# Kernel optimization log

Hardware: AMD Instinct MI355X
Metric: run time of the kernel (lower is better)

The kernel has to match this reference:

```python
import jax, jax.numpy as jnp
import numpy as np

EPS = 1e-5
CG_GROUPS = 4
CG_ALPHA = 2.0

def conv3x3(x, w, stride=1):
    # x: [N,C,H,W], w: [O,I,3,3], padding=1
    return jax.lax.conv_general_dilated(
        x, w, window_strides=(stride, stride), padding=((1, 1), (1, 1)),
        dimension_numbers=('NCHW', 'OIHW', 'NCHW'))

def qconv_cg(x, w, theta):
    # Conditional-gated conv (CGNet-style, wbit=abit=32 -> no quantization):
    # base partial sum from first C/cg_groups input channels, remainder gated
    # by soft sigmoid decision on (Yp - per-channel threshold).
    cin = x.shape[1]
    base = cin // CG_GROUPS  # 64 base channels
    yp = conv3x3(x[:, :base], w[:, :base])          # base partial sum [N,O,H,W]
    yr = conv3x3(x[:, base:], w[:, base:])          # remainder partial sum
    d = jax.nn.sigmoid(CG_ALPHA * (yp - theta[None, :, None, None]))
    return yp + d * yr

def bn(x, gamma, beta, mean, var):
    # inference-mode BatchNorm2d
    inv = gamma * jax.lax.rsqrt(var + EPS)
    return x * inv[None, :, None, None] + (beta - mean * inv)[None, :, None, None]

def setup_inputs() -> dict:
    key = jax.random.key(0)
    k0, k1, k2 = jax.random.split(key, 3)
    C = 256
    x = jax.random.normal(k0, (16, C, 56, 56), jnp.float32)
    scale = 1.0 / np.sqrt(C * 9)
    w_a = jax.random.normal(k1, (C, C, 3, 3), jnp.float32) * scale
    w_b = jax.random.normal(k2, (C, C, 3, 3), jnp.float32) * scale
    z = jnp.zeros((C,), jnp.float32)
    o = jnp.ones((C,), jnp.float32)
    return dict(x=x,
                w_a=w_a, theta_a=z, gamma_a=o, beta_a=z, mean_a=z, var_a=o,
                w_b=w_b, theta_b=z, gamma_b=o, beta_b=z, mean_b=z, var_b=o)

def reference(x, w_a, theta_a, gamma_a, beta_a, mean_a, var_a,
              w_b, theta_b, gamma_b, beta_b, mean_b, var_b):
    h = jax.nn.relu(bn(qconv_cg(x, w_a, theta_a), gamma_a, beta_a, mean_a, var_a))
    h = bn(qconv_cg(h, w_b, theta_b), gamma_b, beta_b, mean_b, var_b)
    return jax.nn.relu(x + h)  # identity residual (downsample=None)
```

## Files before the change

kernel.cpp:

```cpp
#include <hip/hip_runtime.h>
#include <hip/hip_bf16.h>
#include <cstdint>
#include <cstddef>


typedef __attribute__((ext_vector_type(8))) short bf16x8;
typedef __attribute__((ext_vector_type(4))) float f32x4;
typedef __attribute__((ext_vector_type(8))) unsigned short u16x8;

#define HP 58
#define WP 58
#define CIN 256
#define NIMG 16

__device__ __forceinline__ unsigned short f2bf(float f) {
  unsigned int u = __float_as_uint(f);
  u += 0x7fffu + ((u >> 16) & 1u);
  return (unsigned short)(u >> 16);
}

#define GLOAD16(gp, lp)                                                        \
  __builtin_amdgcn_global_load_lds(                                            \
      (const __attribute__((address_space(1))) void*)(gp),                     \
      (__attribute__((address_space(3))) void*)(lp), 16, 0, 0)

__global__ void zero_borders(unsigned short* __restrict__ pad) {
  int b = blockIdx.x;
  int img = b / 58, yp = b - img * 58;
  int tid = threadIdx.x;
  u16x8 z = {0, 0, 0, 0, 0, 0, 0, 0};
  unsigned short* row = pad + ((size_t)(img * HP + yp)) * WP * CIN;
  if (yp == 0 || yp == HP - 1) {
    for (int i = tid; i < WP * CIN / 8; i += 256) ((u16x8*)row)[i] = z;
  } else {
    if (tid < 32) ((u16x8*)row)[tid] = z;
    else if (tid < 64) ((u16x8*)row)[(WP - 1) * CIN / 8 + tid - 32] = z;
  }
}

__global__ void prep_w(const float* __restrict__ wa, const float* __restrict__ wb,
                       unsigned short* __restrict__ bta, unsigned short* __restrict__ btb) {
  int id = blockIdx.x * 256 + threadIdx.x;
  const float* w = (id < 65536) ? wa : wb;
  unsigned short* bt = (id < 65536) ? bta : btb;
  int oi = id & 65535;
  float v[9];
#pragma unroll
  for (int t = 0; t < 9; ++t) v[t] = w[(size_t)oi * 9 + t];
#pragma unroll
  for (int t = 0; t < 9; ++t) bt[(size_t)t * 65536 + oi] = f2bf(v[t]);
}

__global__ void prep_x(const float* __restrict__ x, unsigned short* __restrict__ xpad) {
  __shared__ float ld[56 * 65];
  int b = blockIdx.x;
  int img = b / 56, y = b - img * 56;
  int tid = threadIdx.x;
  for (int cb = 0; cb < 4; ++cb) {
    __syncthreads();
#pragma unroll
    for (int it = 0; it < 14; ++it) {
      int i = tid + it * 256;
      int cl = i / 56, xx = i - cl * 56;
      ld[xx * 65 + cl] = x[((size_t)(img * 256 + cb * 64 + cl) * 56 + y) * 56 + xx];
    }
    __syncthreads();
#pragma unroll
    for (int it = 0; it < 14; ++it) {
      int j = tid + it * 256;
      int xx = j >> 6, c = j & 63;
      xpad[((size_t)((img * HP) + (y + 1)) * WP + (xx + 1)) * CIN + cb * 64 + c] =
          f2bf(ld[xx * 65 + c]);
    }
  }
}

template <int LAYER>
__global__ __launch_bounds__(256, 2)
void conv_cg(const unsigned short* __restrict__ inp,
             const unsigned short* __restrict__ Bt,
             const float* __restrict__ theta,
             const float* __restrict__ gammav,
             const float* __restrict__ betav,
             const float* __restrict__ meanv,
             const float* __restrict__ varv,
             unsigned short* __restrict__ hout,
             const float* __restrict__ xres,
             float* __restrict__ dout)
{
  __shared__ alignas(16) char smem[64 * 129 * 4];
  unsigned short* sA = (unsigned short*)smem;
  unsigned short* sB = (unsigned short*)(smem + 8192);
  float* sep = (float*)smem;

  const int tid = threadIdx.x;
  const int lane = tid & 63;
  const int wid = tid >> 6;
  const int wm = wid >> 1, wn = wid & 1;
  const int l15 = lane & 15, l4 = lane >> 4;
  const int srow = lane >> 3;
  const int sslot = lane & 7;

  int bx = blockIdx.x;
  const int ob = bx & 1; bx >>= 1;
  const int img = bx / 49;
  const int r2 = bx - img * 49;
  const int ty = r2 / 7, tx = r2 - ty * 7;
  const int y0 = ty * 8 + 1, x0 = tx * 8 + 1;

  const size_t img_base = (size_t)img * (HP * WP * CIN);

  f32x4 acc[2][4], ypv[2][4];
  const f32x4 fzero = {0.f, 0.f, 0.f, 0.f};
#pragma unroll
  for (int i = 0; i < 2; ++i)
#pragma unroll
    for (int j = 0; j < 4; ++j) acc[i][j] = fzero;

  for (int phase = 0; phase < 2; ++phase) {
    const int cb_lo = phase ? 1 : 0;
    const int cb_hi = phase ? 4 : 1;
    for (int tap = 0; tap < 9; ++tap) {
      const int dy = tap / 3 - 1, dx = tap - (tap / 3) * 3 - 1;
      for (int cb = cb_lo; cb < cb_hi; ++cb) {
#pragma unroll
        for (int it = 0; it < 2; ++it) {
          int chunk = wid * 2 + it;
          int row = chunk * 8 + srow;
          int ry = row >> 3, rx = row & 7;
          int gy = y0 + ry + dy, gx = x0 + rx + dx;
          int slot = sslot ^ (row & 7);
          const unsigned short* src =
              inp + img_base + ((size_t)(gy * WP + gx)) * CIN + cb * 64 + slot * 8;
          GLOAD16(src, sA + chunk * 512);
        }
#pragma unroll
        for (int it = 0; it < 4; ++it) {
          int chunk = wid * 4 + it;
          int o_l = chunk * 8 + srow;
          int slot = sslot ^ (o_l & 7);
          const unsigned short* src =
              Bt + ((size_t)(tap * 256 + ob * 128 + o_l)) * 256 + cb * 64 + slot * 8;
          GLOAD16(src, sB + chunk * 512);
        }
        __syncthreads();
#pragma unroll
        for (int ks = 0; ks < 2; ++ks) {
          bf16x8 av[2], bv[4];
#pragma unroll
          for (int mi = 0; mi < 2; ++mi) {
            int row = wm * 32 + mi * 16 + l15;
            int sl = (ks * 4 + l4) ^ (row & 7);
            av[mi] = *(const bf16x8*)(sA + row * 64 + sl * 8);
          }
#pragma unroll
          for (int ni = 0; ni < 4; ++ni) {
            int row = wn * 64 + ni * 16 + l15;
            int sl = (ks * 4 + l4) ^ (row & 7);
            bv[ni] = *(const bf16x8*)(sB + row * 64 + sl * 8);
          }
#pragma unroll
          for (int mi = 0; mi < 2; ++mi)
#pragma unroll
            for (int ni = 0; ni < 4; ++ni)
              acc[mi][ni] = __builtin_amdgcn_mfma_f32_16x16x32_bf16(
                  av[mi], bv[ni], acc[mi][ni], 0, 0, 0);
        }
        __syncthreads();
      }
    }
    if (phase == 0) {
#pragma unroll
      for (int i = 0; i < 2; ++i)
#pragma unroll
        for (int j = 0; j < 4; ++j) { ypv[i][j] = acc[i][j]; acc[i][j] = fzero; }
    }
  }

  float th[4], sc[4], bi[4];
#pragma unroll
  for (int ni = 0; ni < 4; ++ni) {
    int o = ob * 128 + wn * 64 + ni * 16 + l15;
    th[ni] = theta[o];
    float inv = gammav[o] * rsqrtf(varv[o] + 1e-5f);
    sc[ni] = inv;
    bi[ni] = betav[o] - meanv[o] * inv;
  }
#pragma unroll
  for (int mi = 0; mi < 2; ++mi)
#pragma unroll
    for (int ni = 0; ni < 4; ++ni) {
      int colL = wn * 64 + ni * 16 + l15;
#pragma unroll
      for (int q = 0; q < 4; ++q) {
        int m = wm * 32 + mi * 16 + l4 * 4 + q;
        float yp = ypv[mi][ni][q], yr = acc[mi][ni][q];
        float d = 1.f / (1.f + __expf(-2.f * (yp - th[ni])));
        float v = (yp + d * yr) * sc[ni] + bi[ni];
        if (LAYER == 1) v = fmaxf(v, 0.f);
        sep[m * 129 + colL] = v;
      }
    }
  __syncthreads();

  if (LAYER == 1) {
#pragma unroll
    for (int it = 0; it < 4; ++it) {
      int j = tid + it * 256;
      int p = j >> 4, o8 = (j & 15) * 8;
      int ry = p >> 3, rx = p & 7;
      u16x8 tv;
#pragma unroll
      for (int e = 0; e < 8; ++e) tv[e] = f2bf(sep[p * 129 + o8 + e]);
      unsigned short* dst =
          hout + img_base + ((size_t)((y0 + ry) * WP + (x0 + rx))) * CIN + ob * 128 + o8;
      *(u16x8*)dst = tv;
    }
  } else {
#pragma unroll
    for (int it = 0; it < 4; ++it) {
      int j = tid + it * 256;
      int o = j >> 3, ry = j & 7;
      int oc = ob * 128 + o;
      size_t gb = ((size_t)((img * 256 + oc) * 56 + (y0 - 1 + ry))) * 56 + (x0 - 1);
      const float4 xa = *(const float4*)(xres + gb);
      const float4 xb = *(const float4*)(xres + gb + 4);
      float4 ra, rb;
      ra.x = fmaxf(xa.x + sep[(ry * 8 + 0) * 129 + o], 0.f);
      ra.y = fmaxf(xa.y + sep[(ry * 8 + 1) * 129 + o], 0.f);
      ra.z = fmaxf(xa.z + sep[(ry * 8 + 2) * 129 + o], 0.f);
      ra.w = fmaxf(xa.w + sep[(ry * 8 + 3) * 129 + o], 0.f);
      rb.x = fmaxf(xb.x + sep[(ry * 8 + 4) * 129 + o], 0.f);
      rb.y = fmaxf(xb.y + sep[(ry * 8 + 5) * 129 + o], 0.f);
      rb.z = fmaxf(xb.z + sep[(ry * 8 + 6) * 129 + o], 0.f);
      rb.w = fmaxf(xb.w + sep[(ry * 8 + 7) * 129 + o], 0.f);
      *(float4*)(dout + gb) = ra;
      *(float4*)(dout + gb + 4) = rb;
    }
  }
}

extern "C" void kernel_launch(void* const* d_in, const int* in_sizes, int n_in,
                              void* d_out, int out_size, void* d_ws, size_t ws_size,
                              hipStream_t stream) {
  const float* x    = (const float*)d_in[0];
  const float* w_a  = (const float*)d_in[1];
  const float* th_a = (const float*)d_in[2];
  const float* ga_a = (const float*)d_in[3];
  const float* be_a = (const float*)d_in[4];
  const float* mu_a = (const float*)d_in[5];
  const float* va_a = (const float*)d_in[6];
  const float* w_b  = (const float*)d_in[7];
  const float* th_b = (const float*)d_in[8];
  const float* ga_b = (const float*)d_in[9];
  const float* be_b = (const float*)d_in[10];
  const float* mu_b = (const float*)d_in[11];
  const float* va_b = (const float*)d_in[12];
  float* out = (float*)d_out;

  const size_t PAD_BYTES = (size_t)NIMG * HP * WP * CIN * 2;
  char* ws = (char*)d_ws;
  unsigned short* xpad = (unsigned short*)ws;
  unsigned short* hpad = (unsigned short*)(ws + 27558912);
  unsigned short* bta  = (unsigned short*)(ws + 2 * 27558912);
  unsigned short* btb  = (unsigned short*)(ws + 2 * 27558912 + 1179648);
  (void)PAD_BYTES; (void)ws_size; (void)in_sizes; (void)n_in; (void)out_size;

  hipLaunchKernelGGL(zero_borders, dim3(NIMG * HP), dim3(256), 0, stream, xpad);
  hipLaunchKernelGGL(zero_borders, dim3(NIMG * HP), dim3(256), 0, stream, hpad);
  hipLaunchKernelGGL(prep_w, dim3(512), dim3(256), 0, stream, w_a, w_b, bta, btb);
  hipLaunchKernelGGL(prep_x, dim3(NIMG * 56), dim3(256), 0, stream, x, xpad);

  hipLaunchKernelGGL((conv_cg<1>), dim3(NIMG * 49 * 2), dim3(256), 0, stream,
                     xpad, bta, th_a, ga_a, be_a, mu_a, va_a,
                     hpad, (const float*)nullptr, (float*)nullptr);
  hipLaunchKernelGGL((conv_cg<2>), dim3(NIMG * 49 * 2), dim3(256), 0, stream,
                     hpad, btb, th_b, ga_b, be_b, mu_b, va_b,
                     (unsigned short*)nullptr, x, out);
}
```

Before: 350.2 us.

## Stage halo input tile once per channel block and double-buffer weights per tap

The conv kernel is restructured so each wave owns one 8x8 pixel tile. It loads a 10x10 halo patch per 64-channel block into LDS once and reuses it across all 9 taps. Before, the input patch was reloaded for every tap. Each block of 4 waves shares a 64-output-channel weight slice, staged per tap with double buffering so the next tap's weights load while MFMAs run. The weight layout is reordered to match, and x-buffer border zeroing is merged into prep_x, removing one launch. In exchange it uses much more LDS (about 66 KB per block), holds 32 accumulator vectors per lane which lowers occupancy, and launches fewer blocks.

```diff
diff --git a/kernel.cpp b/kernel.cpp
--- a/kernel.cpp
+++ b/kernel.cpp
@@ -44,34 +44,60 @@
   const float* w = (id < 65536) ? wa : wb;
   unsigned short* bt = (id < 65536) ? bta : btb;
   int oi = id & 65535;
+  int o = oi >> 8, i = oi & 255;
+  int cb = i >> 6, c = i & 63;
   float v[9];
 #pragma unroll
   for (int t = 0; t < 9; ++t) v[t] = w[(size_t)oi * 9 + t];
 #pragma unroll
-  for (int t = 0; t < 9; ++t) bt[(size_t)t * 65536 + oi] = f2bf(v[t]);
+  for (int t = 0; t < 9; ++t)
+    bt[((size_t)((t * 4 + cb) * 256 + o)) * 64 + c] = f2bf(v[t]);
 }
 
 __global__ void prep_x(const float* __restrict__ x, unsigned short* __restrict__ xpad) {
   __shared__ float ld[56 * 65];
   int b = blockIdx.x;
-  int img = b / 56, y = b - img * 56;
+  int img = b / 58, y = b - img * 58;
   int tid = threadIdx.x;
+  unsigned short* row = xpad + ((size_t)(img * HP + y)) * WP * CIN;
+  u16x8 z = {0, 0, 0, 0, 0, 0, 0, 0};
+  if (y == 0 || y == HP - 1) {
+#pragma unroll
+    for (int it = 0; it < 8; ++it) {
+      int i = it * 256 + tid;
+      if (i < WP * CIN / 8) ((u16x8*)row)[i] = z;
+    }
+    return;
+  }
+  if (tid < 32) ((u16x8*)row)[tid] = z;
+  else if (tid < 64) ((u16x8*)row)[(WP - 1) * CIN / 8 + tid - 32] = z;
+  int ys = y - 1;
   for (int cb = 0; cb < 4; ++cb) {
     __syncthreads();
 #pragma unroll
     for (int it = 0; it < 14; ++it) {
       int i = tid + it * 256;
       int cl = i / 56, xx = i - cl * 56;
-      ld[xx * 65 + cl] = x[((size_t)(img * 256 + cb * 64 + cl) * 56 + y) * 56 + xx];
+      ld[xx * 65 + cl] = x[((size_t)(img * 256 + cb * 64 + cl) * 56 + ys) * 56 + xx];
     }
     __syncthreads();
 #pragma unroll
     for (int it = 0; it < 14; ++it) {
       int j = tid + it * 256;
       int xx = j >> 6, c = j & 63;
-      xpad[((size_t)((img * HP) + (y + 1)) * WP + (xx + 1)) * CIN + cb * 64 + c] =
-          f2bf(ld[xx * 65 + c]);
-    }
+      row[(xx + 1) * CIN + cb * 64 + c] = f2bf(ld[xx * 65 + c]);
+    }
+  }
+}
+
+__device__ __forceinline__ void stage_b(const unsigned short* __restrict__ cbase,
+                                        unsigned short* dst, int wid, int lane) {
+#pragma unroll
+  for (int it = 0; it < 2; ++it) {
+    int d = (wid * 2 + it) * 64 + lane;
+    int o = d >> 3, s = d & 7;
+    const unsigned short* src = cbase + o * 64 + ((s ^ (o & 7)) << 3);
+    GLOAD16(src, dst + (wid * 2 + it) * 512);
   }
 }
 
@@ -88,154 +114,154 @@
              const float* __restrict__ xres,
              float* __restrict__ dout)
 {
-  __shared__ alignas(16) char smem[64 * 129 * 4];
-  unsigned short* sA = (unsigned short*)smem;
-  unsigned short* sB = (unsigned short*)(smem + 8192);
-  float* sep = (float*)smem;
-
+  __shared__ alignas(16) char smem[67584];
   const int tid = threadIdx.x;
   const int lane = tid & 63;
   const int wid = tid >> 6;
-  const int wm = wid >> 1, wn = wid & 1;
   const int l15 = lane & 15, l4 = lane >> 4;
-  const int srow = lane >> 3;
-  const int sslot = lane & 7;
 
   int bx = blockIdx.x;
-  const int ob = bx & 1; bx >>= 1;
-  const int img = bx / 49;
-  const int r2 = bx - img * 49;
-  const int ty = r2 / 7, tx = r2 - ty * 7;
+  const int oq = bx & 3;
+  const int pxg = bx >> 2;
+  const int tile = pxg * 4 + wid;
+  const int img = tile / 49;
+  const int rr = tile - img * 49;
+  const int ty = rr / 7, tx = rr - ty * 7;
   const int y0 = ty * 8 + 1, x0 = tx * 8 + 1;
-
   const size_t img_base = (size_t)img * (HP * WP * CIN);
 
-  f32x4 acc[2][4], ypv[2][4];
-  const f32x4 fzero = {0.f, 0.f, 0.f, 0.f};
-#pragma unroll
-  for (int i = 0; i < 2; ++i)
-#pragma unroll
-    for (int j = 0; j < 4; ++j) acc[i][j] = fzero;
-
-  for (int phase = 0; phase < 2; ++phase) {
-    const int cb_lo = phase ? 1 : 0;
-    const int cb_hi = phase ? 4 : 1;
-    for (int tap = 0; tap < 9; ++tap) {
-      const int dy = tap / 3 - 1, dx = tap - (tap / 3) * 3 - 1;
-      for (int cb = cb_lo; cb < cb_hi; ++cb) {
-#pragma unroll
-        for (int it = 0; it < 2; ++it) {
-          int chunk = wid * 2 + it;
-          int row = chunk * 8 + srow;
-          int ry = row >> 3, rx = row & 7;
-          int gy = y0 + ry + dy, gx = x0 + rx + dx;
-          int slot = sslot ^ (row & 7);
-          const unsigned short* src =
-              inp + img_base + ((size_t)(gy * WP + gx)) * CIN + cb * 64 + slot * 8;
-          GLOAD16(src, sA + chunk * 512);
-        }
-#pragma unroll
-        for (int it = 0; it < 4; ++it) {
-          int chunk = wid * 4 + it;
-          int o_l = chunk * 8 + srow;
-          int slot = sslot ^ (o_l & 7);
-          const unsigned short* src =
-              Bt + ((size_t)(tap * 256 + ob * 128 + o_l)) * 256 + cb * 64 + slot * 8;
-          GLOAD16(src, sB + chunk * 512);
-        }
-        __syncthreads();
-#pragma unroll
-        for (int ks = 0; ks < 2; ++ks) {
-          bf16x8 av[2], bv[4];
-#pragma unroll
-          for (int mi = 0; mi < 2; ++mi) {
-            int row = wm * 32 + mi * 16 + l15;
-            int sl = (ks * 4 + l4) ^ (row & 7);
-            av[mi] = *(const bf16x8*)(sA + row * 64 + sl * 8);
-          }
-#pragma unroll
-          for (int ni = 0; ni < 4; ++ni) {
-            int row = wn * 64 + ni * 16 + l15;
-            int sl = (ks * 4 + l4) ^ (row & 7);
-            bv[ni] = *(const bf16x8*)(sB + row * 64 + sl * 8);
-          }
-#pragma unroll
-          for (int mi = 0; mi < 2; ++mi)
-#pragma unroll
-            for (int ni = 0; ni < 4; ++ni)
-              acc[mi][ni] = __builtin_amdgcn_mfma_f32_16x16x32_bf16(
-                  av[mi], bv[ni], acc[mi][ni], 0, 0, 0);
-        }
-        __syncthreads();
-      }
-    }
-    if (phase == 0) {
-#pragma unroll
-      for (int i = 0; i < 2; ++i)
-#pragma unroll
-        for (int j = 0; j < 4; ++j) { ypv[i][j] = acc[i][j]; acc[i][j] = fzero; }
-    }
-  }
+  unsigned short* sAw = (unsigned short*)smem + wid * 6400;
+  unsigned short* sB0 = (unsigned short*)(smem + 51200);
+  unsigned short* sB1 = (unsigned short*)(smem + 59392);
 
   float th[4], sc[4], bi[4];
 #pragma unroll
   for (int ni = 0; ni < 4; ++ni) {
-    int o = ob * 128 + wn * 64 + ni * 16 + l15;
+    int o = oq * 64 + ni * 16 + l15;
     th[ni] = theta[o];
     float inv = gammav[o] * rsqrtf(varv[o] + 1e-5f);
     sc[ni] = inv;
     bi[ni] = betav[o] - meanv[o] * inv;
   }
-#pragma unroll
-  for (int mi = 0; mi < 2; ++mi)
-#pragma unroll
-    for (int ni = 0; ni < 4; ++ni) {
-      int colL = wn * 64 + ni * 16 + l15;
-#pragma unroll
-      for (int q = 0; q < 4; ++q) {
-        int m = wm * 32 + mi * 16 + l4 * 4 + q;
-        float yp = ypv[mi][ni][q], yr = acc[mi][ni][q];
-        float d = 1.f / (1.f + __expf(-2.f * (yp - th[ni])));
-        float v = (yp + d * yr) * sc[ni] + bi[ni];
-        if (LAYER == 1) v = fmaxf(v, 0.f);
-        sep[m * 129 + colL] = v;
-      }
-    }
-  __syncthreads();
-
-  if (LAYER == 1) {
-#pragma unroll
-    for (int it = 0; it < 4; ++it) {
-      int j = tid + it * 256;
-      int p = j >> 4, o8 = (j & 15) * 8;
-      int ry = p >> 3, rx = p & 7;
-      u16x8 tv;
-#pragma unroll
-      for (int e = 0; e < 8; ++e) tv[e] = f2bf(sep[p * 129 + o8 + e]);
-      unsigned short* dst =
-          hout + img_base + ((size_t)((y0 + ry) * WP + (x0 + rx))) * CIN + ob * 128 + o8;
-      *(u16x8*)dst = tv;
-    }
-  } else {
-#pragma unroll
-    for (int it = 0; it < 4; ++it) {
-      int j = tid + it * 256;
-      int o = j >> 3, ry = j & 7;
-      int oc = ob * 128 + o;
-      size_t gb = ((size_t)((img * 256 + oc) * 56 + (y0 - 1 + ry))) * 56 + (x0 - 1);
-      const float4 xa = *(const float4*)(xres + gb);
-      const float4 xb = *(const float4*)(xres + gb + 4);
-      float4 ra, rb;
-      ra.x = fmaxf(xa.x + sep[(ry * 8 + 0) * 129 + o], 0.f);
-      ra.y = fmaxf(xa.y + sep[(ry * 8 + 1) * 129 + o], 0.f);
-      ra.z = fmaxf(xa.z + sep[(ry * 8 + 2) * 129 + o], 0.f);
-      ra.w = fmaxf(xa.w + sep[(ry * 8 + 3) * 129 + o], 0.f);
-      rb.x = fmaxf(xb.x + sep[(ry * 8 + 4) * 129 + o], 0.f);
-      rb.y = fmaxf(xb.y + sep[(ry * 8 + 5) * 129 + o], 0.f);
-      rb.z = fmaxf(xb.z + sep[(ry * 8 + 6) * 129 + o], 0.f);
-      rb.w = fmaxf(xb.w + sep[(ry * 8 + 7) * 129 + o], 0.f);
-      *(float4*)(dout + gb) = ra;
-      *(float4*)(dout + gb + 4) = rb;
+
+  f32x4 acc[4][4], ypv[4][4];
+  const f32x4 fzero = {0.f, 0.f, 0.f, 0.f};
+#pragma unroll
+  for (int i = 0; i < 4; ++i)
+#pragma unroll
+    for (int j = 0; j < 4; ++j) { acc[i][j] = fzero; ypv[i][j] = fzero; }
+
+  for (int cb = 0; cb < 4; ++cb) {
+    {
+      const unsigned short* abase = inp + img_base + cb * 64;
+#pragma unroll
+      for (int it = 0; it < 13; ++it) {
+        int v = it * 64 + lane;
+        if (v < 800) {
+          int ppx = v >> 3, s = v & 7;
+          int py = ppx / 10, pxx = ppx - py * 10;
+          const unsigned short* src = abase +
+              ((size_t)((y0 - 1 + py) * WP + (x0 - 1 + pxx))) * CIN +
+              ((s ^ (ppx & 7)) << 3);
+          GLOAD16(src, sAw + it * 512);
+        }
+      }
+    }
+    stage_b(Bt + ((size_t)((0 * 4 + cb) * 256 + oq * 64)) * 64, sB0, wid, lane);
+    __syncthreads();
+
+#pragma unroll
+    for (int tap = 0; tap < 9; ++tap) {
+      if (tap < 8) {
+        unsigned short* nb = ((tap + 1) & 1) ? sB1 : sB0;
+        stage_b(Bt + ((size_t)(((tap + 1) * 4 + cb) * 256 + oq * 64)) * 64,
+                nb, wid, lane);
+      }
+      const unsigned short* bb = (tap & 1) ? sB1 : sB0;
+      const int dy = tap / 3 - 1, dxx = tap - (tap / 3) * 3 - 1;
+#pragma unroll
+      for (int ks = 0; ks < 2; ++ks) {
+        bf16x8 av[4], bv[4];
+#pragma unroll
+        for (int mi = 0; mi < 4; ++mi) {
+          int ry = mi * 2 + (l15 >> 3);
+          int ppx = (ry + dy + 1) * 10 + (l15 & 7) + dxx + 1;
+          av[mi] = *(const bf16x8*)(sAw + ppx * 64 +
+                                    (((ks * 4 + l4) ^ (ppx & 7)) << 3));
+        }
+#pragma unroll
+        for (int ni = 0; ni < 4; ++ni) {
+          int ol = ni * 16 + l15;
+          bv[ni] = *(const bf16x8*)(bb + ol * 64 +
+                                    (((ks * 4 + l4) ^ (ol & 7)) << 3));
+        }
+#pragma unroll
+        for (int mi = 0; mi < 4; ++mi)
+#pragma unroll
+          for (int ni = 0; ni < 4; ++ni)
+            acc[mi][ni] = __builtin_amdgcn_mfma_f32_16x16x32_bf16(
+                av[mi], bv[ni], acc[mi][ni], 0, 0, 0);
+      }
+      __syncthreads();
+    }
+    if (cb == 0) {
+#pragma unroll
+      for (int i = 0; i < 4; ++i)
+#pragma unroll
+        for (int j = 0; j < 4; ++j) { ypv[i][j] = acc[i][j]; acc[i][j] = fzero; }
+    }
+  }
+
+  float* sep = (float*)smem + wid * 2176;
+#pragma unroll
+  for (int r = 0; r < 2; ++r) {
+    __syncthreads();
+#pragma unroll
+    for (int mh = 0; mh < 2; ++mh) {
+      int mi = r * 2 + mh;
+#pragma unroll
+      for (int ni = 0; ni < 4; ++ni)
+#pragma unroll
+        for (int q = 0; q < 4; ++q) {
+          int rowl = mh * 16 + l4 * 4 + q;
+          float yp = ypv[mi][ni][q], yr = acc[mi][ni][q];
+          float dg = 1.f / (1.f + __expf(-2.f * (yp - th[ni])));
+          float v = (yp + dg * yr) * sc[ni] + bi[ni];
+          if (LAYER == 1) v = fmaxf(v, 0.f);
+          sep[rowl * 68 + ni * 16 + l15] = v;
+        }
+    }
+    __syncthreads();
+    if (LAYER == 1) {
+#pragma unroll
+      for (int it = 0; it < 4; ++it) {
+        int u = it * 64 + lane;
+        int pxl = u >> 3, s = u & 7;
+        int m = r * 32 + pxl;
+        int ry = m >> 3, rx = m & 7;
+        u16x8 tv;
+#pragma unroll
+        for (int e = 0; e < 8; ++e) tv[e] = f2bf(sep[pxl * 68 + s * 8 + e]);
+        *(u16x8*)(hout + img_base +
+                  ((size_t)((y0 + ry) * WP + (x0 + rx))) * CIN + oq * 64 + s * 8) = tv;
+      }
+    } else {
+#pragma unroll
+      for (int it = 0; it < 8; ++it) {
+        int idx = it * 64 + lane;
+        int oc = idx >> 3, t = idx & 7;
+        int row4 = t >> 1, half = t & 1;
+        int pxl = row4 * 8 + half * 4;
+        int gy = y0 - 1 + r * 4 + row4, gx = x0 - 1 + half * 4;
+        size_t gb = ((size_t)(img * 256 + oq * 64 + oc) * 56 + gy) * 56 + gx;
+        const float4 xa = *(const float4*)(xres + gb);
+        float4 o4;
+        o4.x = fmaxf(xa.x + sep[(pxl + 0) * 68 + oc], 0.f);
+        o4.y = fmaxf(xa.y + sep[(pxl + 1) * 68 + oc], 0.f);
+        o4.z = fmaxf(xa.z + sep[(pxl + 2) * 68 + oc], 0.f);
+        o4.w = fmaxf(xa.w + sep[(pxl + 3) * 68 + oc], 0.f);
+        *(float4*)(dout + gb) = o4;
+      }
     }
   }
 }
@@ -258,23 +284,21 @@
   const float* va_b = (const float*)d_in[12];
   float* out = (float*)d_out;
 
-  const size_t PAD_BYTES = (size_t)NIMG * HP * WP * CIN * 2;
   char* ws = (char*)d_ws;
   unsigned short* xpad = (unsigned short*)ws;
   unsigned short* hpad = (unsigned short*)(ws + 27558912);
   unsigned short* bta  = (unsigned short*)(ws + 2 * 27558912);
   unsigned short* btb  = (unsigned short*)(ws + 2 * 27558912 + 1179648);
-  (void)PAD_BYTES; (void)ws_size; (void)in_sizes; (void)n_in; (void)out_size;
-
-  hipLaunchKernelGGL(zero_borders, dim3(NIMG * HP), dim3(256), 0, stream, xpad);
+  (void)ws_size; (void)in_sizes; (void)n_in; (void)out_size;
+
   hipLaunchKernelGGL(zero_borders, dim3(NIMG * HP), dim3(256), 0, stream, hpad);
   hipLaunchKernelGGL(prep_w, dim3(512), dim3(256), 0, stream, w_a, w_b, bta, btb);
-  hipLaunchKernelGGL(prep_x, dim3(NIMG * 56), dim3(256), 0, stream, x, xpad);
-
-  hipLaunchKernelGGL((conv_cg<1>), dim3(NIMG * 49 * 2), dim3(256), 0, stream,
+  hipLaunchKernelGGL(prep_x, dim3(NIMG * HP), dim3(256), 0, stream, x, xpad);
+
+  hipLaunchKernelGGL((conv_cg<1>), dim3(784), dim3(256), 0, stream,
                      xpad, bta, th_a, ga_a, be_a, mu_a, va_a,
                      hpad, (const float*)nullptr, (float*)nullptr);
-  hipLaunchKernelGGL((conv_cg<2>), dim3(NIMG * 49 * 2), dim3(256), 0, stream,
+  hipLaunchKernelGGL((conv_cg<2>), dim3(784), dim3(256), 0, stream,
                      hpad, btb, th_b, ga_b, be_b, mu_b, va_b,
                      (unsigned short*)nullptr, x, out);
 }
```

Result: faster. 320.6 us (-8.5%).
